# Kernel tuning notes

Measured on AMD Instinct MI355X. Metric: run time of the kernel, lower is better.

The kernel has to match this reference:

```python
import jax, jax.numpy as jnp
import numpy as np
from jax import lax

K = 11  # AvgPool kernel
PAD = 5
EPS = 1e-5


def _box_avg(x):
    # Separable 11x11 box filter, stride 1, zero padding (count_include_pad=True)
    # x: [B, C, H, W]
    s = lax.reduce_window(x, 0.0, lax.add, (1, 1, K, 1), (1, 1, 1, 1),
                          [(0, 0), (0, 0), (PAD, PAD), (0, 0)])
    s = lax.reduce_window(s, 0.0, lax.add, (1, 1, 1, K), (1, 1, 1, 1),
                          [(0, 0), (0, 0), (0, 0), (PAD, PAD)])
    return s * (1.0 / (K * K))


def _bn(x, g, b, m, v):
    # eval-mode BatchNorm2d over channel dim (axis 1)
    scale = (g / jnp.sqrt(v + EPS))[None, :, None, None]
    shift = (b - m * g / jnp.sqrt(v + EPS))[None, :, None, None]
    return x * scale + shift


def setup_inputs() -> dict:
    key = jax.random.key(0)
    ks = jax.random.split(key, 13)
    B, C, H, W = 16, 256, 128, 128
    Ch = C // 2
    return {
        "x": jax.random.normal(ks[0], (B, C, H, W), jnp.float32),
        "w1": jax.random.normal(ks[1], (Ch, C), jnp.float32) * (1.0 / np.sqrt(C)),
        "b1": jax.random.normal(ks[2], (Ch,), jnp.float32) * 0.1,
        "bn1_g": jax.random.uniform(ks[3], (Ch,), jnp.float32, 0.5, 1.5),
        "bn1_b": jax.random.normal(ks[4], (Ch,), jnp.float32) * 0.1,
        "bn1_m": jax.random.normal(ks[5], (Ch,), jnp.float32) * 0.1,
        "bn1_v": jax.random.uniform(ks[6], (Ch,), jnp.float32, 0.5, 1.5),
        "w2": jax.random.normal(ks[7], (C, Ch), jnp.float32) * (1.0 / np.sqrt(Ch)),
        "b2": jax.random.normal(ks[8], (C,), jnp.float32) * 0.1,
        "bn2_g": jax.random.uniform(ks[9], (C,), jnp.float32, 0.5, 1.5),
        "bn2_b": jax.random.normal(ks[10], (C,), jnp.float32) * 0.1,
        "bn2_m": jax.random.normal(ks[11], (C,), jnp.float32) * 0.1,
        "bn2_v": jax.random.uniform(ks[12], (C,), jnp.float32, 0.5, 1.5),
    }


def reference(x, w1, b1, bn1_g, bn1_b, bn1_m, bn1_v,
              w2, b2, bn2_g, bn2_b, bn2_m, bn2_v):
    # edge features: high-pass via box-filter subtraction
    edge = x - _box_avg(x)
    # 1x1 conv -> BN -> ReLU
    h = jnp.einsum('bchw,oc->bohw', edge, w1) + b1[None, :, None, None]
    h = jax.nn.relu(_bn(h, bn1_g, bn1_b, bn1_m, bn1_v))
    # 1x1 conv -> BN -> Sigmoid
    w = jnp.einsum('bchw,oc->bohw', h, w2) + b2[None, :, None, None]
    w = jax.nn.sigmoid(_bn(w, bn2_g, bn2_b, bn2_m, bn2_v))
    # gated residual enhancement
    return w * x + x
```

## Files before the change

### kernel.cpp

```cpp
#include <hip/hip_runtime.h>

#define BB 16
#define CC 256
#define CH 128
#define HH 128
#define WW 128
#define HW (HH*WW)
#define KPOOL 11
#define PADP 5
#define EPS 1e-5f

typedef __attribute__((ext_vector_type(8))) short s16x8;
typedef __attribute__((ext_vector_type(4))) float f32x4;
typedef __attribute__((ext_vector_type(8))) unsigned short u16x8;
typedef __attribute__((ext_vector_type(4))) unsigned short u16x4;
typedef __attribute__((ext_vector_type(4))) unsigned int u32x4;

static __device__ __forceinline__ unsigned short f2bf(float f) {
    unsigned int u = __float_as_uint(f);
    u = u + 0x7fffu + ((u >> 16) & 1u);
    return (unsigned short)(u >> 16);
}
static __device__ __forceinline__ float bf2f(unsigned short h) {
    return __uint_as_float(((unsigned int)h) << 16);
}

#define MFMA16(a, b, c) __builtin_amdgcn_mfma_f32_16x16x32_bf16((a), (b), (c), 0, 0, 0)

__global__ __launch_bounds__(256) void prep_kernel(
    const float* __restrict__ w1, const float* __restrict__ b1,
    const float* __restrict__ g1, const float* __restrict__ be1,
    const float* __restrict__ m1, const float* __restrict__ v1,
    const float* __restrict__ w2, const float* __restrict__ b2,
    const float* __restrict__ g2, const float* __restrict__ be2,
    const float* __restrict__ m2, const float* __restrict__ v2,
    unsigned short* __restrict__ w1h, unsigned short* __restrict__ w1l,
    unsigned short* __restrict__ w2h, unsigned short* __restrict__ w2l,
    float* __restrict__ A1, float* __restrict__ B1,
    float* __restrict__ A2, float* __restrict__ B2)
{
    int i = blockIdx.x * 256 + threadIdx.x;
    if (i < CH * CC) {
        float w = w1[i];
        unsigned short hi = f2bf(w);
        w1h[i] = hi;
        w1l[i] = f2bf(w - bf2f(hi));
        float u = w2[i];
        unsigned short hi2 = f2bf(u);
        w2h[i] = hi2;
        w2l[i] = f2bf(u - bf2f(hi2));
    }
    if (i < CH) {
        float sc = g1[i] * rsqrtf(v1[i] + EPS);
        A1[i] = sc;
        B1[i] = be1[i] + (b1[i] - m1[i]) * sc;
    }
    if (i < CC) {
        float sc = g2[i] * rsqrtf(v2[i] + EPS);
        A2[i] = sc;
        B2[i] = be2[i] + (b2[i] - m2[i]) * sc;
    }
}

__global__ __launch_bounds__(256) void box_edge_kernel(
    const float* __restrict__ x, unsigned short* __restrict__ edge)
{
    constexpr int RB = 16;
    int blk  = blockIdx.x;
    int band = blk & 7;
    int bc   = blk >> 3;
    const float* img = x + (size_t)bc * HW;

    __shared__ float tile[RB + 2*PADP][WW];
    __shared__ float vs[RB][WW];

    int h0 = band * RB;

    for (int idx = threadIdx.x; idx < (RB + 2*PADP) * (WW/4); idx += blockDim.x) {
        int r  = idx >> 5;
        int w4 = idx & 31;
        int h  = h0 - PADP + r;
        f32x4 v = {0.f, 0.f, 0.f, 0.f};
        if (h >= 0 && h < HH) v = *(const f32x4*)(img + h * WW + w4 * 4);
        *(f32x4*)&tile[r][w4 * 4] = v;
    }
    __syncthreads();

    for (int idx = threadIdx.x; idx < RB * WW; idx += blockDim.x) {
        int r = idx >> 7;
        int w = idx & 127;
        float s = 0.f;
#pragma unroll
        for (int j = 0; j < KPOOL; ++j) s += tile[r + j][w];
        vs[r][w] = s;
    }
    __syncthreads();

    for (int idx = threadIdx.x; idx < RB * WW; idx += blockDim.x) {
        int r = idx >> 7;
        int w = idx & 127;
        float s = 0.f;
#pragma unroll
        for (int dx = -PADP; dx <= PADP; ++dx) {
            int ww = w + dx;
            if (ww >= 0 && ww < WW) s += vs[r][ww];
        }
        float e = tile[r + PADP][w] - s * (1.f / (KPOOL * KPOOL));
        edge[(size_t)bc * HW + (size_t)(h0 + r) * WW + w] = f2bf(e);
    }
}

__global__ __launch_bounds__(256) void transpose_kernel(
    const unsigned short* __restrict__ edge_raw, unsigned short* __restrict__ edge_t)
{
    int blk = blockIdx.x;
    int c0 = (blk & 3) * 64;
    int p0 = ((blk >> 2) & 255) * 64;
    int b  = blk >> 10;

    __shared__ unsigned int lds32[64 * 33];

    int t  = threadIdx.x;
    int rp = t >> 3;
    int sl = t & 7;

    size_t rowA = ((size_t)(b * CC + c0 + 2 * rp)) << 14;
    u16x8 a = *(const u16x8*)(edge_raw + rowA + p0 + sl * 8);
    u16x8 c = *(const u16x8*)(edge_raw + rowA + (1 << 14) + p0 + sl * 8);

#pragma unroll
    for (int j = 0; j < 8; ++j) {
        unsigned int w = (unsigned int)a[j] | ((unsigned int)c[j] << 16);
        lds32[(sl * 8 + j) * 33 + rp] = w;
    }
    __syncthreads();

    int p = t >> 2;
    int q = t & 3;
    u32x4 o0, o1;
#pragma unroll
    for (int k = 0; k < 4; ++k) o0[k] = lds32[p * 33 + q * 8 + k];
#pragma unroll
    for (int k = 0; k < 4; ++k) o1[k] = lds32[p * 33 + q * 8 + 4 + k];

    unsigned short* dst = edge_t + (((size_t)(b * HW + p0 + p)) << 8) + c0 + q * 16;
    *(u32x4*)dst       = o0;
    *(u32x4*)(dst + 8) = o1;
}

__global__ __launch_bounds__(256, 4) void gemm12_fused(
    const unsigned short* __restrict__ edge_t,
    const unsigned short* __restrict__ w1h, const unsigned short* __restrict__ w1l,
    const float* __restrict__ A1, const float* __restrict__ B1,
    const unsigned short* __restrict__ w2h, const unsigned short* __restrict__ w2l,
    const float* __restrict__ A2, const float* __restrict__ B2,
    const float* __restrict__ x, float* __restrict__ out)
{
    const int blk  = blockIdx.x;
    const int b    = blk >> 8;
    const int p0   = (blk & 255) * 64;
    const int tid  = threadIdx.x;
    const int lane = tid & 63;
    const int l15  = lane & 15;
    const int l4   = lane >> 4;
    const int wv   = tid >> 6;

    __shared__ unsigned short hT[64 * 128];

    const unsigned short* E = edge_t + (((size_t)(b * HW + p0)) << 8);

    const f32x4 z4 = {0.f, 0.f, 0.f, 0.f};

    {
        const int o0 = wv * 32;
        f32x4 acc[2][4];
#pragma unroll
        for (int fo = 0; fo < 2; ++fo)
#pragma unroll
            for (int fp = 0; fp < 4; ++fp) acc[fo][fp] = z4;

#pragma unroll
        for (int ks = 0; ks < 8; ++ks) {
            s16x8 bfr[4];
#pragma unroll
            for (int fp = 0; fp < 4; ++fp) {
                int pl = fp * 16 + l15;
                bfr[fp] = *(const s16x8*)(E + ((size_t)pl << 8) + ks * 32 + l4 * 8);
            }
#pragma unroll
            for (int fo = 0; fo < 2; ++fo) {
                int o = o0 + fo * 16 + l15;
                size_t wo = (size_t)o * CC + ks * 32 + l4 * 8;
                s16x8 ah = *(const s16x8*)(w1h + wo);
                s16x8 al = *(const s16x8*)(w1l + wo);
#pragma unroll
                for (int fp = 0; fp < 4; ++fp) {
                    acc[fo][fp] = MFMA16(ah, bfr[fp], acc[fo][fp]);
                    acc[fo][fp] = MFMA16(al, bfr[fp], acc[fo][fp]);
                }
            }
        }

#pragma unroll
        for (int fo = 0; fo < 2; ++fo) {
            int ob = o0 + fo * 16 + l4 * 4;
            f32x4 sc = *(const f32x4*)(A1 + ob);
            f32x4 sh = *(const f32x4*)(B1 + ob);
#pragma unroll
            for (int fp = 0; fp < 4; ++fp) {
                int pl = fp * 16 + l15;
                u16x4 hv;
#pragma unroll
                for (int r = 0; r < 4; ++r) {
                    float v = acc[fo][fp][r] * sc[r] + sh[r];
                    v = fmaxf(v, 0.f);
                    hv[r] = f2bf(v);
                }
                *(u16x4*)&hT[pl * 128 + ((ob >> 3) ^ (pl & 7)) * 8 + (ob & 7)] = hv;
            }
        }
    }
    __syncthreads();

    {
        const int o0 = wv * 64;
        f32x4 acc[4][4];
#pragma unroll
        for (int fo = 0; fo < 4; ++fo)
#pragma unroll
            for (int fp = 0; fp < 4; ++fp) acc[fo][fp] = z4;

#pragma unroll
        for (int ks = 0; ks < 4; ++ks) {
            s16x8 bfr[4];
#pragma unroll
            for (int fp = 0; fp < 4; ++fp) {
                int pl = fp * 16 + l15;
                int g  = ks * 4 + l4;
                bfr[fp] = *(const s16x8*)&hT[pl * 128 + (g ^ (pl & 7)) * 8];
            }
#pragma unroll
            for (int fo = 0; fo < 4; ++fo) {
                int o = o0 + fo * 16 + l15;
                size_t wo = (size_t)o * CH + ks * 32 + l4 * 8;
                s16x8 ah = *(const s16x8*)(w2h + wo);
                s16x8 al = *(const s16x8*)(w2l + wo);
#pragma unroll
                for (int fp = 0; fp < 4; ++fp) {
                    acc[fo][fp] = MFMA16(ah, bfr[fp], acc[fo][fp]);
                    acc[fo][fp] = MFMA16(al, bfr[fp], acc[fo][fp]);
                }
            }
        }

#pragma unroll
        for (int fo = 0; fo < 4; ++fo) {
            int ob = o0 + fo * 16 + l4 * 4;
            f32x4 sc = *(const f32x4*)(A2 + ob);
            f32x4 sh = *(const f32x4*)(B2 + ob);
#pragma unroll
            for (int fp = 0; fp < 4; ++fp) {
                int p = p0 + fp * 16 + l15;
#pragma unroll
                for (int r = 0; r < 4; ++r) {
                    float z = acc[fo][fp][r] * sc[r] + sh[r];
                    float gte = 1.f / (1.f + __expf(-z));
                    size_t idx = (((size_t)(b * CC + ob + r)) << 14) + p;
                    out[idx] = x[idx] * (1.f + gte);
                }
            }
        }
    }
}

extern "C" void kernel_launch(void* const* d_in, const int* in_sizes, int n_in,
                              void* d_out, int out_size, void* d_ws, size_t ws_size,
                              hipStream_t stream) {
    const float* x   = (const float*)d_in[0];
    const float* w1  = (const float*)d_in[1];
    const float* b1  = (const float*)d_in[2];
    const float* g1  = (const float*)d_in[3];
    const float* be1 = (const float*)d_in[4];
    const float* m1  = (const float*)d_in[5];
    const float* v1  = (const float*)d_in[6];
    const float* w2  = (const float*)d_in[7];
    const float* b2  = (const float*)d_in[8];
    const float* g2  = (const float*)d_in[9];
    const float* be2 = (const float*)d_in[10];
    const float* m2  = (const float*)d_in[11];
    const float* v2  = (const float*)d_in[12];
    float* out = (float*)d_out;

    const size_t EDGE_BYTES  = (size_t)BB * CC * HW * 2;
    const size_t SMALL_BYTES = 4 * (size_t)CH * CC * 2 + (2 * CH + 2 * CC) * 4;

    unsigned short* edge_raw = (unsigned short*)d_out;
    unsigned short* edge_t;
    char* smalls;
    if (ws_size >= EDGE_BYTES + SMALL_BYTES) {
        edge_t = (unsigned short*)d_ws;
        smalls = (char*)d_ws + EDGE_BYTES;
    } else {
        edge_t = (unsigned short*)((char*)d_out + EDGE_BYTES);
        smalls = (char*)d_ws;
    }
    unsigned short* w1h = (unsigned short*)smalls;
    unsigned short* w1l = w1h + CH * CC;
    unsigned short* w2h = w1l + CH * CC;
    unsigned short* w2l = w2h + CH * CC;
    float* A1v = (float*)(w2l + CH * CC);
    float* B1v = A1v + CH;
    float* A2v = B1v + CH;
    float* B2v = A2v + CC;

    prep_kernel<<<128, 256, 0, stream>>>(w1, b1, g1, be1, m1, v1,
                                         w2, b2, g2, be2, m2, v2,
                                         w1h, w1l, w2h, w2l, A1v, B1v, A2v, B2v);

    box_edge_kernel<<<BB * CC * (HH / 16), 256, 0, stream>>>(x, edge_raw);

    transpose_kernel<<<BB * (HW / 64) * (CC / 64), 256, 0, stream>>>(edge_raw, edge_t);

    gemm12_fused<<<BB * (HW / 64), 256, 0, stream>>>(
        edge_t, w1h, w1l, A1v, B1v, w2h, w2l, A2v, B2v, x, out);
}
```

Baseline: 855.1 us.

## Fuse box-filter edge computation with channel-major transpose; split GEMM2 epilogue passes

Result: slower. 950.3 us (+11.1%).

```diff
diff --git a/kernel.cpp b/kernel.cpp
--- a/kernel.cpp
+++ b/kernel.cpp
@@ -14,7 +14,6 @@
 typedef __attribute__((ext_vector_type(4))) float f32x4;
 typedef __attribute__((ext_vector_type(8))) unsigned short u16x8;
 typedef __attribute__((ext_vector_type(4))) unsigned short u16x4;
-typedef __attribute__((ext_vector_type(4))) unsigned int u32x4;
 
 static __device__ __forceinline__ unsigned short f2bf(float f) {
     unsigned int u = __float_as_uint(f);
@@ -62,93 +61,74 @@
     }
 }
 
-__global__ __launch_bounds__(256) void box_edge_kernel(
-    const float* __restrict__ x, unsigned short* __restrict__ edge)
+__global__ __launch_bounds__(256) void box_edge_t_kernel(
+    const float* __restrict__ x, unsigned int* __restrict__ edge_t32)
 {
     constexpr int RB = 16;
-    int blk  = blockIdx.x;
-    int band = blk & 7;
-    int bc   = blk >> 3;
-    const float* img = x + (size_t)bc * HW;
+    int L  = blockIdx.x;
+    int wg = (L & 7) * 2048 + (L >> 3);
+    int cpair = wg & 127;
+    int band  = (wg >> 7) & 7;
+    int b     = wg >> 10;
+    int h0    = band * RB;
 
     __shared__ float tile[RB + 2*PADP][WW];
     __shared__ float vs[RB][WW];
 
-    int h0 = band * RB;
-
-    for (int idx = threadIdx.x; idx < (RB + 2*PADP) * (WW/4); idx += blockDim.x) {
-        int r  = idx >> 5;
-        int w4 = idx & 31;
-        int h  = h0 - PADP + r;
-        f32x4 v = {0.f, 0.f, 0.f, 0.f};
-        if (h >= 0 && h < HH) v = *(const f32x4*)(img + h * WW + w4 * 4);
-        *(f32x4*)&tile[r][w4 * 4] = v;
-    }
-    __syncthreads();
-
-    for (int idx = threadIdx.x; idx < RB * WW; idx += blockDim.x) {
-        int r = idx >> 7;
-        int w = idx & 127;
-        float s = 0.f;
-#pragma unroll
-        for (int j = 0; j < KPOOL; ++j) s += tile[r + j][w];
-        vs[r][w] = s;
-    }
-    __syncthreads();
-
-    for (int idx = threadIdx.x; idx < RB * WW; idx += blockDim.x) {
-        int r = idx >> 7;
-        int w = idx & 127;
-        float s = 0.f;
-#pragma unroll
-        for (int dx = -PADP; dx <= PADP; ++dx) {
-            int ww = w + dx;
-            if (ww >= 0 && ww < WW) s += vs[r][ww];
-        }
-        float e = tile[r + PADP][w] - s * (1.f / (KPOOL * KPOOL));
-        edge[(size_t)bc * HW + (size_t)(h0 + r) * WW + w] = f2bf(e);
-    }
-}
-
-__global__ __launch_bounds__(256) void transpose_kernel(
-    const unsigned short* __restrict__ edge_raw, unsigned short* __restrict__ edge_t)
-{
-    int blk = blockIdx.x;
-    int c0 = (blk & 3) * 64;
-    int p0 = ((blk >> 2) & 255) * 64;
-    int b  = blk >> 10;
-
-    __shared__ unsigned int lds32[64 * 33];
-
-    int t  = threadIdx.x;
-    int rp = t >> 3;
-    int sl = t & 7;
-
-    size_t rowA = ((size_t)(b * CC + c0 + 2 * rp)) << 14;
-    u16x8 a = *(const u16x8*)(edge_raw + rowA + p0 + sl * 8);
-    u16x8 c = *(const u16x8*)(edge_raw + rowA + (1 << 14) + p0 + sl * 8);
-
-#pragma unroll
-    for (int j = 0; j < 8; ++j) {
-        unsigned int w = (unsigned int)a[j] | ((unsigned int)c[j] << 16);
-        lds32[(sl * 8 + j) * 33 + rp] = w;
-    }
-    __syncthreads();
-
-    int p = t >> 2;
-    int q = t & 3;
-    u32x4 o0, o1;
-#pragma unroll
-    for (int k = 0; k < 4; ++k) o0[k] = lds32[p * 33 + q * 8 + k];
-#pragma unroll
-    for (int k = 0; k < 4; ++k) o1[k] = lds32[p * 33 + q * 8 + 4 + k];
-
-    unsigned short* dst = edge_t + (((size_t)(b * HW + p0 + p)) << 8) + c0 + q * 16;
-    *(u32x4*)dst       = o0;
-    *(u32x4*)(dst + 8) = o1;
-}
-
-__global__ __launch_bounds__(256, 4) void gemm12_fused(
+    unsigned short eo[2][8];
+
+#pragma unroll
+    for (int cp = 0; cp < 2; ++cp) {
+        int c = cpair * 2 + cp;
+        const float* img = x + (size_t)(b * CC + c) * HW;
+        if (cp) __syncthreads();
+
+        for (int idx = threadIdx.x; idx < (RB + 2*PADP) * (WW/4); idx += 256) {
+            int r  = idx >> 5;
+            int w4 = idx & 31;
+            int h  = h0 - PADP + r;
+            f32x4 v = {0.f, 0.f, 0.f, 0.f};
+            if (h >= 0 && h < HH) v = *(const f32x4*)(img + h * WW + w4 * 4);
+            *(f32x4*)&tile[r][w4 * 4] = v;
+        }
+        __syncthreads();
+
+        for (int idx = threadIdx.x; idx < RB * WW; idx += 256) {
+            int r = idx >> 7;
+            int w = idx & 127;
+            float s = 0.f;
+#pragma unroll
+            for (int j = 0; j < KPOOL; ++j) s += tile[r + j][w];
+            vs[r][w] = s;
+        }
+        __syncthreads();
+
+#pragma unroll
+        for (int i = 0; i < 8; ++i) {
+            int idx = threadIdx.x + i * 256;
+            int r = idx >> 7;
+            int w = idx & 127;
+            float s = 0.f;
+#pragma unroll
+            for (int dx = -PADP; dx <= PADP; ++dx) {
+                int ww = w + dx;
+                if (ww >= 0 && ww < WW) s += vs[r][ww];
+            }
+            float e = tile[r + PADP][w] - s * (1.f / (KPOOL * KPOOL));
+            eo[cp][i] = f2bf(e);
+        }
+    }
+
+    size_t base = (size_t)b * HW + (size_t)h0 * WW;
+#pragma unroll
+    for (int i = 0; i < 8; ++i) {
+        int idx = threadIdx.x + i * 256;
+        unsigned int wv = (unsigned int)eo[0][i] | ((unsigned int)eo[1][i] << 16);
+        edge_t32[(base + idx) * 128 + cpair] = wv;
+    }
+}
+
+__global__ __launch_bounds__(256, 5) void gemm12_fused(
     const unsigned short* __restrict__ edge_t,
     const unsigned short* __restrict__ w1h, const unsigned short* __restrict__ w1l,
     const float* __restrict__ A1, const float* __restrict__ B1,
@@ -222,11 +202,12 @@
     }
     __syncthreads();
 
-    {
-        const int o0 = wv * 64;
-        f32x4 acc[4][4];
-#pragma unroll
-        for (int fo = 0; fo < 4; ++fo)
+#pragma unroll
+    for (int pass = 0; pass < 2; ++pass) {
+        const int o0 = wv * 64 + pass * 32;
+        f32x4 acc[2][4];
+#pragma unroll
+        for (int fo = 0; fo < 2; ++fo)
 #pragma unroll
             for (int fp = 0; fp < 4; ++fp) acc[fo][fp] = z4;
 
@@ -240,7 +221,7 @@
                 bfr[fp] = *(const s16x8*)&hT[pl * 128 + (g ^ (pl & 7)) * 8];
             }
 #pragma unroll
-            for (int fo = 0; fo < 4; ++fo) {
+            for (int fo = 0; fo < 2; ++fo) {
                 int o = o0 + fo * 16 + l15;
                 size_t wo = (size_t)o * CH + ks * 32 + l4 * 8;
                 s16x8 ah = *(const s16x8*)(w2h + wo);
@@ -254,7 +235,7 @@
         }
 
 #pragma unroll
-        for (int fo = 0; fo < 4; ++fo) {
+        for (int fo = 0; fo < 2; ++fo) {
             int ob = o0 + fo * 16 + l4 * 4;
             f32x4 sc = *(const f32x4*)(A2 + ob);
             f32x4 sh = *(const f32x4*)(B2 + ob);
@@ -294,7 +275,6 @@
     const size_t EDGE_BYTES  = (size_t)BB * CC * HW * 2;
     const size_t SMALL_BYTES = 4 * (size_t)CH * CC * 2 + (2 * CH + 2 * CC) * 4;
 
-    unsigned short* edge_raw = (unsigned short*)d_out;
     unsigned short* edge_t;
     char* smalls;
     if (ws_size >= EDGE_BYTES + SMALL_BYTES) {
@@ -317,9 +297,8 @@
                                          w2, b2, g2, be2, m2, v2,
                                          w1h, w1l, w2h, w2l, A1v, B1v, A2v, B2v);
 
-    box_edge_kernel<<<BB * CC * (HH / 16), 256, 0, stream>>>(x, edge_raw);
-
-    transpose_kernel<<<BB * (HW / 64) * (CC / 64), 256, 0, stream>>>(edge_raw, edge_t);
+    box_edge_t_kernel<<<BB * (HH / 16) * (CC / 2), 256, 0, stream>>>(
+        x, (unsigned int*)edge_t);
 
     gemm12_fused<<<BB * (HW / 64), 256, 0, stream>>>(
         edge_t, w1h, w1l, A1v, B1v, w2h, w2l, A2v, B2v, x, out);
```

## Stage edge tile in LDS and double gemm block to eight waves

Applied to the files above, without the earlier changes.

New measurement: 813.9 us. 4.8% less time.

```diff
diff --git a/kernel.cpp b/kernel.cpp
--- a/kernel.cpp
+++ b/kernel.cpp
@@ -148,7 +148,7 @@
     *(u32x4*)(dst + 8) = o1;
 }
 
-__global__ __launch_bounds__(256, 4) void gemm12_fused(
+__global__ __launch_bounds__(512, 6) void gemm12_fused(
     const unsigned short* __restrict__ edge_t,
     const unsigned short* __restrict__ w1h, const unsigned short* __restrict__ w1l,
     const float* __restrict__ A1, const float* __restrict__ B1,
@@ -165,11 +165,64 @@
     const int l4   = lane >> 4;
     const int wv   = tid >> 6;
 
+    __shared__ unsigned short eT[64 * 256];
     __shared__ unsigned short hT[64 * 128];
 
     const unsigned short* E = edge_t + (((size_t)(b * HW + p0)) << 8);
 
+#pragma unroll
+    for (int i = 0; i < 4; ++i) {
+        int L  = i * 512 + tid;
+        int pl = L >> 5;
+        int s  = L & 31;
+        int g  = s ^ (pl & 7);
+        *(u16x8*)&eT[pl * 256 + s * 8] = *(const u16x8*)(E + pl * 256 + g * 8);
+    }
+    __syncthreads();
+
     const f32x4 z4 = {0.f, 0.f, 0.f, 0.f};
+
+    {
+        const int o = wv * 16 + l15;
+        f32x4 acc[4];
+#pragma unroll
+        for (int fp = 0; fp < 4; ++fp) acc[fp] = z4;
+
+#pragma unroll
+        for (int ks = 0; ks < 8; ++ks) {
+            s16x8 bfr[4];
+#pragma unroll
+            for (int fp = 0; fp < 4; ++fp) {
+                int pl = fp * 16 + l15;
+                bfr[fp] = *(const s16x8*)&eT[pl * 256 + ((ks * 4 + l4) ^ (pl & 7)) * 8];
+            }
+            size_t wo = (size_t)o * CC + ks * 32 + l4 * 8;
+            s16x8 ah = *(const s16x8*)(w1h + wo);
+            s16x8 al = *(const s16x8*)(w1l + wo);
+#pragma unroll
+            for (int fp = 0; fp < 4; ++fp) {
+                acc[fp] = MFMA16(ah, bfr[fp], acc[fp]);
+                acc[fp] = MFMA16(al, bfr[fp], acc[fp]);
+            }
+        }
+
+        int ob = wv * 16 + l4 * 4;
+        f32x4 sc = *(const f32x4*)(A1 + ob);
+        f32x4 sh = *(const f32x4*)(B1 + ob);
+#pragma unroll
+        for (int fp = 0; fp < 4; ++fp) {
+            int pl = fp * 16 + l15;
+            u16x4 hv;
+#pragma unroll
+            for (int r = 0; r < 4; ++r) {
+                float v = acc[fp][r] * sc[r] + sh[r];
+                v = fmaxf(v, 0.f);
+                hv[r] = f2bf(v);
+            }
+            *(u16x4*)&hT[pl * 128 + ((ob >> 3) ^ (pl & 7)) * 8 + (ob & 7)] = hv;
+        }
+    }
+    __syncthreads();
 
     {
         const int o0 = wv * 32;
@@ -180,19 +233,19 @@
             for (int fp = 0; fp < 4; ++fp) acc[fo][fp] = z4;
 
 #pragma unroll
-        for (int ks = 0; ks < 8; ++ks) {
+        for (int ks = 0; ks < 4; ++ks) {
             s16x8 bfr[4];
 #pragma unroll
             for (int fp = 0; fp < 4; ++fp) {
                 int pl = fp * 16 + l15;
-                bfr[fp] = *(const s16x8*)(E + ((size_t)pl << 8) + ks * 32 + l4 * 8);
+                bfr[fp] = *(const s16x8*)&hT[pl * 128 + ((ks * 4 + l4) ^ (pl & 7)) * 8];
             }
 #pragma unroll
             for (int fo = 0; fo < 2; ++fo) {
                 int o = o0 + fo * 16 + l15;
-                size_t wo = (size_t)o * CC + ks * 32 + l4 * 8;
-                s16x8 ah = *(const s16x8*)(w1h + wo);
-                s16x8 al = *(const s16x8*)(w1l + wo);
+                size_t wo = (size_t)o * CH + ks * 32 + l4 * 8;
+                s16x8 ah = *(const s16x8*)(w2h + wo);
+                s16x8 al = *(const s16x8*)(w2l + wo);
 #pragma unroll
                 for (int fp = 0; fp < 4; ++fp) {
                     acc[fo][fp] = MFMA16(ah, bfr[fp], acc[fo][fp]);
@@ -203,58 +256,6 @@
 
 #pragma unroll
         for (int fo = 0; fo < 2; ++fo) {
-            int ob = o0 + fo * 16 + l4 * 4;
-            f32x4 sc = *(const f32x4*)(A1 + ob);
-            f32x4 sh = *(const f32x4*)(B1 + ob);
-#pragma unroll
-            for (int fp = 0; fp < 4; ++fp) {
-                int pl = fp * 16 + l15;
-                u16x4 hv;
-#pragma unroll
-                for (int r = 0; r < 4; ++r) {
-                    float v = acc[fo][fp][r] * sc[r] + sh[r];
-                    v = fmaxf(v, 0.f);
-                    hv[r] = f2bf(v);
-                }
-                *(u16x4*)&hT[pl * 128 + ((ob >> 3) ^ (pl & 7)) * 8 + (ob & 7)] = hv;
-            }
-        }
-    }
-    __syncthreads();
-
-    {
-        const int o0 = wv * 64;
-        f32x4 acc[4][4];
-#pragma unroll
-        for (int fo = 0; fo < 4; ++fo)
-#pragma unroll
-            for (int fp = 0; fp < 4; ++fp) acc[fo][fp] = z4;
-
-#pragma unroll
-        for (int ks = 0; ks < 4; ++ks) {
-            s16x8 bfr[4];
-#pragma unroll
-            for (int fp = 0; fp < 4; ++fp) {
-                int pl = fp * 16 + l15;
-                int g  = ks * 4 + l4;
-                bfr[fp] = *(const s16x8*)&hT[pl * 128 + (g ^ (pl & 7)) * 8];
-            }
-#pragma unroll
-            for (int fo = 0; fo < 4; ++fo) {
-                int o = o0 + fo * 16 + l15;
-                size_t wo = (size_t)o * CH + ks * 32 + l4 * 8;
-                s16x8 ah = *(const s16x8*)(w2h + wo);
-                s16x8 al = *(const s16x8*)(w2l + wo);
-#pragma unroll
-                for (int fp = 0; fp < 4; ++fp) {
-                    acc[fo][fp] = MFMA16(ah, bfr[fp], acc[fo][fp]);
-                    acc[fo][fp] = MFMA16(al, bfr[fp], acc[fo][fp]);
-                }
-            }
-        }
-
-#pragma unroll
-        for (int fo = 0; fo < 4; ++fo) {
             int ob = o0 + fo * 16 + l4 * 4;
             f32x4 sc = *(const f32x4*)(A2 + ob);
             f32x4 sh = *(const f32x4*)(B2 + ob);
@@ -321,6 +322,6 @@
 
     transpose_kernel<<<BB * (HW / 64) * (CC / 64), 256, 0, stream>>>(edge_raw, edge_t);
 
-    gemm12_fused<<<BB * (HW / 64), 256, 0, stream>>>(
+    gemm12_fused<<<BB * (HW / 64), 512, 0, stream>>>(
         edge_t, w1h, w1l, A1v, B1v, w2h, w2l, A2v, B2v, x, out);
 }
```
